# Optimization experiments

Measured on AMD Instinct MI355X. Metric: run time of the kernel, lower is better.

## Reference

```python
import jax, jax.numpy as jnp
import numpy as np

B, H, K, D = 4096, 3, 32768, 128


def setup_inputs() -> dict:
    key = jax.random.key(0)
    k_in, k_emb = jax.random.split(key)
    inputs = jax.random.normal(k_in, (B, 1, D), dtype=jnp.float32)
    # xavier-uniform-ish init with per-head decay 0.5**h (gain 6.0), as in the module
    ks = jax.random.split(k_emb, H)
    tables = []
    for h in range(H):
        gain = 6.0 * (0.5 ** h)
        bound = gain * np.sqrt(6.0 / (K + D))
        tables.append(jax.random.uniform(ks[h], (K, D), jnp.float32, -bound, bound))
    emb = jnp.stack(tables, axis=0)  # [H, K, D]
    return {"inputs": inputs, "emb": emb}


def reference(inputs, emb):
    # Eval-mode HRQ forward: per-head negative squared-L2 distances to the
    # codebook on the running residual, hard argmax assignment, summed codes.
    x = inputs[:, 0, :]                      # [B, D]
    n_heads = emb.shape[0]
    resid = x
    quantized = jnp.zeros_like(x)
    codes = []
    for h in range(n_heads):
        W = emb[h]                            # [K, D]
        # -(||r||^2 + ||w||^2 - 2 r.w)  -> argmax == nearest code
        dists = -(jnp.sum(resid * resid, axis=1, keepdims=True)
                  + jnp.sum(W * W, axis=1)
                  - 2.0 * resid @ W.T)        # [B, K]
        c = jnp.argmax(dists, axis=-1)        # [B]
        q = jnp.take(W, c, axis=0)            # onehot(c) @ W == gather
        resid = resid - q
        quantized = quantized + q
        codes.append(c)
    loss = jnp.zeros(x.shape[0], dtype=inputs.dtype)
    return loss, quantized.reshape(inputs.shape), jnp.stack(codes, axis=1)
```

## Files before the change

kernel.cpp:

```cpp
#include <hip/hip_runtime.h>
#include <math.h>

#define NB 4096
#define NH 3
#define NK 32768
#define ND 128
#define KA 256
#define KB 256
#define RB 64
#define CS 32
#define CPB (NK / CS)
#define CI 256
#define NCI (CPB / CI)

typedef _Float16 half8_t __attribute__((ext_vector_type(8)));
typedef _Float16 half2_t __attribute__((ext_vector_type(2)));
typedef float f32x4 __attribute__((ext_vector_type(4)));
typedef __attribute__((address_space(1))) const unsigned int gu32_t;
typedef __attribute__((address_space(3))) unsigned int lu32_t;

__global__ __launch_bounds__(64) void init_kernel(const float* __restrict__ inp,
                                                  float* __restrict__ resid,
                                                  float* __restrict__ rr,
                                                  float* __restrict__ out,
                                                  _Float16* __restrict__ Aext) {
  int row = blockIdx.x;
  int lane = threadIdx.x;
  const float2* ip = (const float2*)(inp + row * ND);
  float2 v = ip[lane];
  ((float2*)(resid + row * ND))[lane] = v;
  ((float2*)(out + NB + row * ND))[lane] = make_float2(0.f, 0.f);
  if (lane == 0) out[row] = 0.f;
  _Float16 h0 = (_Float16)v.x, h1 = (_Float16)v.y;
  _Float16 l0 = (_Float16)(v.x - (float)h0), l1 = (_Float16)(v.y - (float)h1);
  half2_t h = {h0, h1}, l = {l0, l1};
  _Float16* base = Aext + (size_t)row * KA;
  *(half2_t*)(base + 2 * lane) = h;
  *(half2_t*)(base + 128 + 2 * lane) = l;
  float s = v.x * v.x + v.y * v.y;
  #pragma unroll
  for (int m = 32; m; m >>= 1) s += __shfl_xor(s, m, 64);
  if (lane == 0) rr[row] = s;
}

__global__ __launch_bounds__(256) void norms_kernel(const float* __restrict__ emb,
                                                    float* __restrict__ norms) {
  int row = blockIdx.x * 4 + (threadIdx.x >> 6);
  int lane = threadIdx.x & 63;
  const float2* wp = (const float2*)(emb + (size_t)row * ND);
  float2 v = wp[lane];
  float s = v.x * v.x + v.y * v.y;
  #pragma unroll
  for (int m = 32; m; m >>= 1) s += __shfl_xor(s, m, 64);
  if (lane == 0) norms[row] = s;
}

__global__ __launch_bounds__(256) void split_w_all_kernel(const float* __restrict__ emb,
                                                          _Float16* __restrict__ Bext) {
  const int head = blockIdx.x >> 11;
  const int cg = blockIdx.x & 2047;
  const int n_lo = threadIdx.x & 15;
  const int c = threadIdx.x >> 4;
  const int n = cg * 16 + n_lo;

  const float4* wp = (const float4*)(emb + (size_t)head * NK * ND + (size_t)n * ND + c * 8);
  float4 v0 = wp[0], v1 = wp[1];
  float xv[8] = {v0.x, v0.y, v0.z, v0.w, v1.x, v1.y, v1.z, v1.w};
  half8_t h, l;
  #pragma unroll
  for (int j = 0; j < 8; ++j) {
    _Float16 hh = (_Float16)xv[j];
    h[j] = hh;
    l[j] = (_Float16)(xv[j] - (float)hh);
  }
  const int ks0 = c >> 2;
  const int klo = c & 3;
  _Float16* base = Bext + (size_t)head * NK * KB + (size_t)(cg >> 2) * 16384 +
                   (cg & 3) * 512 + klo * 128 + n_lo * 8;
  *(half8_t*)(base + ks0 * 2048) = h;
  *(half8_t*)(base + (4 + ks0) * 2048) = l;
}

__global__ __launch_bounds__(256, 2) void score_mfma_kernel(
    const _Float16* __restrict__ Aext, const _Float16* __restrict__ Bext,
    const float* __restrict__ rr, const float* __restrict__ normh,
    float* __restrict__ partial_s, int* __restrict__ partial_i) {
  __shared__ __align__(16) _Float16 Ash[RB * KA];

  const int bid = blockIdx.x;
  const int cs = bid & (CS - 1);
  const int rowb = bid / CS;
  const int rowBase = rowb * RB;
  const int colBase0 = cs * CPB;

  const int tid = threadIdx.x;
  const int lane = tid & 63;
  const int wn = tid >> 6;
  const int l15 = lane & 15;
  const int q = lane >> 4;

  {
    const int mrow = lane >> 3;
    const int cg = (lane & 7) ^ (mrow & 7);
    #pragma unroll
    for (int i = 0; i < 8; ++i) {
      int wc = wn * 8 + i;
      int p = wc >> 3;
      int m0 = (wc & 7) * 8;
      const _Float16* gA = Aext + (size_t)(rowBase + m0 + mrow) * KA + p * 64 + cg * 8;
      __builtin_amdgcn_global_load_lds((gu32_t*)gA, (lu32_t*)&Ash[(p * 64 + m0) * 64], 16, 0, 0);
    }
  }

  int aaddr[2][4];
  #pragma unroll
  for (int par = 0; par < 2; ++par)
    #pragma unroll
    for (int mt = 0; mt < 4; ++mt) {
      int m = mt * 16 + l15;
      int slot = (par * 4 + q) ^ (m & 7);
      aaddr[par][mt] = (m * 8 + slot) * 16;
    }

  float rv[16];
  #pragma unroll
  for (int mt = 0; mt < 4; ++mt)
    #pragma unroll
    for (int reg = 0; reg < 4; ++reg)
      rv[mt * 4 + reg] = rr[rowBase + mt * 16 + q * 4 + reg];

  float bs[16];
  int bi[16];
  #pragma unroll
  for (int t = 0; t < 16; ++t) { bs[t] = -INFINITY; bi[t] = 0x7fffffff; }

  __syncthreads();

  #pragma unroll 1
  for (int ci = NCI - 1; ci >= 0; --ci) {
    const int ncol = colBase0 + ci * CI + wn * 64;
    const unsigned int boff = (unsigned int)(ncol >> 6) * 16384u + (unsigned int)lane * 8u;

    float nw[4];
    #pragma unroll
    for (int tn = 0; tn < 4; ++tn) nw[tn] = normh[ncol + tn * 16 + l15];

    f32x4 acc[4][4];
    #pragma unroll
    for (int i = 0; i < 4; ++i)
      #pragma unroll
      for (int j = 0; j < 4; ++j) acc[i][j] = (f32x4){0.f, 0.f, 0.f, 0.f};

    #pragma unroll 2
    for (int kc = 0; kc < 4; ++kc) {
      half8_t bh[4], bl[4];
      #pragma unroll
      for (int tn = 0; tn < 4; ++tn) {
        bh[tn] = *(const half8_t*)(Bext + boff + (unsigned int)(kc * 2048 + tn * 512));
        bl[tn] = *(const half8_t*)(Bext + boff + (unsigned int)((4 + kc) * 2048 + tn * 512));
      }
      const int par = kc & 1, p = kc >> 1;
      half8_t afh[4], afl[4];
      #pragma unroll
      for (int mt = 0; mt < 4; ++mt) {
        afh[mt] = *(const half8_t*)((const char*)Ash + aaddr[par][mt] + p * 8192);
        afl[mt] = *(const half8_t*)((const char*)Ash + aaddr[par][mt] + 16384 + p * 8192);
      }
      #pragma unroll
      for (int mt = 0; mt < 4; ++mt)
        #pragma unroll
        for (int tn = 0; tn < 4; ++tn)
          acc[mt][tn] = __builtin_amdgcn_mfma_f32_16x16x32_f16(afh[mt], bh[tn], acc[mt][tn], 0, 0, 0);
      #pragma unroll
      for (int mt = 0; mt < 4; ++mt)
        #pragma unroll
        for (int tn = 0; tn < 4; ++tn)
          acc[mt][tn] = __builtin_amdgcn_mfma_f32_16x16x32_f16(afl[mt], bh[tn], acc[mt][tn], 0, 0, 0);
      #pragma unroll
      for (int mt = 0; mt < 4; ++mt)
        #pragma unroll
        for (int tn = 0; tn < 4; ++tn)
          acc[mt][tn] = __builtin_amdgcn_mfma_f32_16x16x32_f16(afh[mt], bl[tn], acc[mt][tn], 0, 0, 0);
    }

    #pragma unroll
    for (int tn = 3; tn >= 0; --tn) {
      float nwv = nw[tn];
      int cidx = ncol + tn * 16 + l15;
      #pragma unroll
      for (int mt = 0; mt < 4; ++mt) {
        #pragma unroll
        for (int reg = 0; reg < 4; ++reg) {
          const int s = mt * 4 + reg;
          float t1 = rv[s] + nwv;
          float v = fmaf(2.0f, acc[mt][tn][reg], -t1);
          if (v >= bs[s]) { bs[s] = v; bi[s] = cidx; }
        }
      }
    }
  }

  __syncthreads();
  float* red_s = (float*)Ash;
  int* red_i = (int*)Ash + RB * 4;
  #pragma unroll
  for (int t = 0; t < 16; ++t) {
    float s = bs[t];
    int ii = bi[t];
    #pragma unroll
    for (int mask = 1; mask <= 8; mask <<= 1) {
      float os = __shfl_xor(s, mask, 64);
      int oi = __shfl_xor(ii, mask, 64);
      if (os > s || (os == s && oi < ii)) { s = os; ii = oi; }
    }
    if (l15 == 0) {
      int rloc = (t >> 2) * 16 + q * 4 + (t & 3);
      red_s[rloc * 4 + wn] = s;
      red_i[rloc * 4 + wn] = ii;
    }
  }
  __syncthreads();
  if (tid < RB) {
    float s0 = red_s[tid * 4];
    int i0 = red_i[tid * 4];
    #pragma unroll
    for (int x = 1; x < 4; ++x) {
      float sx = red_s[tid * 4 + x];
      int ix = red_i[tid * 4 + x];
      if (sx > s0 || (sx == s0 && ix < i0)) { s0 = sx; i0 = ix; }
    }
    partial_s[(size_t)(rowBase + tid) * CS + cs] = s0;
    partial_i[(size_t)(rowBase + tid) * CS + cs] = i0;
  }
}

__global__ __launch_bounds__(64) void reduce_update_kernel(const float* __restrict__ embh,
                                                           float* __restrict__ resid,
                                                           float* __restrict__ rr,
                                                           const float* __restrict__ ps,
                                                           const int* __restrict__ pi,
                                                           float* __restrict__ out,
                                                           _Float16* __restrict__ Aext, int h) {
  int row = blockIdx.x;
  int lane = threadIdx.x;
  float bs = -INFINITY;
  int bi = 0x7fffffff;
  if (lane < CS) {
    bs = ps[(size_t)row * CS + lane];
    bi = pi[(size_t)row * CS + lane];
  }
  #pragma unroll
  for (int m = CS >> 1; m; m >>= 1) {
    float os = __shfl_xor(bs, m, 64);
    int oi = __shfl_xor(bi, m, 64);
    if (os > bs || (os == bs && oi < bi)) { bs = os; bi = oi; }
  }
  int c = __shfl(bi, 0, 64);
  if (lane == 0) out[NB + NB * ND + row * NH + h] = (float)c;

  const float* wv = embh + (size_t)c * ND;
  float q0 = wv[lane], q1 = wv[lane + 64];
  float r0 = resid[row * ND + lane] - q0;
  float r1 = resid[row * ND + lane + 64] - q1;
  resid[row * ND + lane] = r0;
  resid[row * ND + lane + 64] = r1;
  out[NB + row * ND + lane] += q0;
  out[NB + row * ND + lane + 64] += q1;

  _Float16 h0 = (_Float16)r0, l0 = (_Float16)(r0 - (float)h0);
  _Float16 h1 = (_Float16)r1, l1 = (_Float16)(r1 - (float)h1);
  _Float16* ab = Aext + (size_t)row * KA;
  ab[lane] = h0;       ab[lane + 64] = h1;
  ab[128 + lane] = l0; ab[128 + lane + 64] = l1;

  float s = r0 * r0 + r1 * r1;
  #pragma unroll
  for (int m = 32; m; m >>= 1) s += __shfl_xor(s, m, 64);
  if (lane == 0) rr[row] = s;
}

extern "C" void kernel_launch(void* const* d_in, const int* in_sizes, int n_in,
                              void* d_out, int out_size, void* d_ws, size_t ws_size,
                              hipStream_t stream) {
  const float* inp = (const float*)d_in[0];
  const float* emb = (const float*)d_in[1];
  float* out = (float*)d_out;

  float* resid = (float*)d_ws;
  float* rr = resid + NB * ND;
  float* norms = rr + NB;
  float* ps = norms + NH * NK;
  int* pi = (int*)(ps + (size_t)NB * CS);
  _Float16* Aext = (_Float16*)(pi + (size_t)NB * CS);
  _Float16* Bext = Aext + (size_t)NB * KA;

  hipLaunchKernelGGL(init_kernel, dim3(NB), dim3(64), 0, stream, inp, resid, rr, out, Aext);
  hipLaunchKernelGGL(norms_kernel, dim3(NH * NK / 4), dim3(256), 0, stream, emb, norms);
  hipLaunchKernelGGL(split_w_all_kernel, dim3(NH * NK / 16), dim3(256), 0, stream, emb, Bext);
  for (int h = 0; h < NH; ++h) {
    hipLaunchKernelGGL(score_mfma_kernel, dim3((NB / RB) * CS), dim3(256), 0, stream,
                       Aext, Bext + (size_t)h * NK * KB, rr, norms + (size_t)h * NK, ps, pi);
    hipLaunchKernelGGL(reduce_update_kernel, dim3(NB), dim3(64), 0, stream,
                       emb + (size_t)h * NK * ND, resid, rr, ps, pi, out, Aext, h);
  }
}
```

Baseline: 438.5 us.

## Shrink per-wave column tile to raise occupancy in score kernel

Each wave now covers 32 codebook columns per iteration instead of 64, which halves the accumulator registers, and launch bounds go from 2 to 4 blocks per SM. The column-split count drops from 32 to 16, so each block scans more columns and fewer partial results need reducing. The first k-chunk is peeled so its MFMAs start from a zero accumulator, and the k loop is fully unrolled. The aim is more latency hiding through occupancy, at the cost of fewer MFMAs per B load and a larger share of LDS A-fragment reloads per column.

```diff
diff --git a/kernel.cpp b/kernel.cpp
--- a/kernel.cpp
+++ b/kernel.cpp
@@ -8,9 +8,9 @@
 #define KA 256
 #define KB 256
 #define RB 64
-#define CS 32
+#define CS 16
 #define CPB (NK / CS)
-#define CI 256
+#define CI 128
 #define NCI (CPB / CI)
 
 typedef _Float16 half8_t __attribute__((ext_vector_type(8)));
@@ -81,7 +81,7 @@
   *(half8_t*)(base + (4 + ks0) * 2048) = l;
 }
 
-__global__ __launch_bounds__(256, 2) void score_mfma_kernel(
+__global__ __launch_bounds__(256, 4) void score_mfma_kernel(
     const _Float16* __restrict__ Aext, const _Float16* __restrict__ Bext,
     const float* __restrict__ rr, const float* __restrict__ normh,
     float* __restrict__ partial_s, int* __restrict__ partial_i) {
@@ -136,26 +136,56 @@
 
   __syncthreads();
 
+  const f32x4 Z = {0.f, 0.f, 0.f, 0.f};
+
   #pragma unroll 1
   for (int ci = NCI - 1; ci >= 0; --ci) {
-    const int ncol = colBase0 + ci * CI + wn * 64;
-    const unsigned int boff = (unsigned int)(ncol >> 6) * 16384u + (unsigned int)lane * 8u;
-
-    float nw[4];
-    #pragma unroll
-    for (int tn = 0; tn < 4; ++tn) nw[tn] = normh[ncol + tn * 16 + l15];
-
-    f32x4 acc[4][4];
-    #pragma unroll
-    for (int i = 0; i < 4; ++i)
-      #pragma unroll
-      for (int j = 0; j < 4; ++j) acc[i][j] = (f32x4){0.f, 0.f, 0.f, 0.f};
-
-    #pragma unroll 2
-    for (int kc = 0; kc < 4; ++kc) {
-      half8_t bh[4], bl[4];
-      #pragma unroll
-      for (int tn = 0; tn < 4; ++tn) {
+    const int ncol = colBase0 + ci * CI + wn * 32;
+    const unsigned int boff = (unsigned int)(ncol >> 6) * 16384u +
+                              ((unsigned int)(ncol >> 4) & 3u) * 512u +
+                              (unsigned int)lane * 8u;
+
+    float nw[2];
+    #pragma unroll
+    for (int tn = 0; tn < 2; ++tn) nw[tn] = normh[ncol + tn * 16 + l15];
+
+    f32x4 acc[4][2];
+
+    {
+      half8_t bh[2], bl[2];
+      #pragma unroll
+      for (int tn = 0; tn < 2; ++tn) {
+        bh[tn] = *(const half8_t*)(Bext + boff + (unsigned int)(tn * 512));
+        bl[tn] = *(const half8_t*)(Bext + boff + (unsigned int)(4 * 2048 + tn * 512));
+      }
+      half8_t afh[4], afl[4];
+      #pragma unroll
+      for (int mt = 0; mt < 4; ++mt) {
+        afh[mt] = *(const half8_t*)((const char*)Ash + aaddr[0][mt]);
+        afl[mt] = *(const half8_t*)((const char*)Ash + aaddr[0][mt] + 16384);
+      }
+      #pragma unroll
+      for (int mt = 0; mt < 4; ++mt)
+        #pragma unroll
+        for (int tn = 0; tn < 2; ++tn)
+          acc[mt][tn] = __builtin_amdgcn_mfma_f32_16x16x32_f16(afh[mt], bh[tn], Z, 0, 0, 0);
+      #pragma unroll
+      for (int mt = 0; mt < 4; ++mt)
+        #pragma unroll
+        for (int tn = 0; tn < 2; ++tn)
+          acc[mt][tn] = __builtin_amdgcn_mfma_f32_16x16x32_f16(afl[mt], bh[tn], acc[mt][tn], 0, 0, 0);
+      #pragma unroll
+      for (int mt = 0; mt < 4; ++mt)
+        #pragma unroll
+        for (int tn = 0; tn < 2; ++tn)
+          acc[mt][tn] = __builtin_amdgcn_mfma_f32_16x16x32_f16(afh[mt], bl[tn], acc[mt][tn], 0, 0, 0);
+    }
+
+    #pragma unroll
+    for (int kc = 1; kc < 4; ++kc) {
+      half8_t bh[2], bl[2];
+      #pragma unroll
+      for (int tn = 0; tn < 2; ++tn) {
         bh[tn] = *(const half8_t*)(Bext + boff + (unsigned int)(kc * 2048 + tn * 512));
         bl[tn] = *(const half8_t*)(Bext + boff + (unsigned int)((4 + kc) * 2048 + tn * 512));
       }
@@ -169,22 +199,22 @@
       #pragma unroll
       for (int mt = 0; mt < 4; ++mt)
         #pragma unroll
-        for (int tn = 0; tn < 4; ++tn)
+        for (int tn = 0; tn < 2; ++tn)
           acc[mt][tn] = __builtin_amdgcn_mfma_f32_16x16x32_f16(afh[mt], bh[tn], acc[mt][tn], 0, 0, 0);
       #pragma unroll
       for (int mt = 0; mt < 4; ++mt)
         #pragma unroll
-        for (int tn = 0; tn < 4; ++tn)
+        for (int tn = 0; tn < 2; ++tn)
           acc[mt][tn] = __builtin_amdgcn_mfma_f32_16x16x32_f16(afl[mt], bh[tn], acc[mt][tn], 0, 0, 0);
       #pragma unroll
       for (int mt = 0; mt < 4; ++mt)
         #pragma unroll
-        for (int tn = 0; tn < 4; ++tn)
+        for (int tn = 0; tn < 2; ++tn)
           acc[mt][tn] = __builtin_amdgcn_mfma_f32_16x16x32_f16(afh[mt], bl[tn], acc[mt][tn], 0, 0, 0);
     }
 
     #pragma unroll
-    for (int tn = 3; tn >= 0; --tn) {
+    for (int tn = 1; tn >= 0; --tn) {
       float nwv = nw[tn];
       int cidx = ncol + tn * 16 + l15;
       #pragma unroll
```

Measured after the change: 1.184 ms. +170.1%, slower.
